# Performance work log

Hardware: AMD Instinct MI355X
Metric: run time of the kernel (lower is better)

Reference implementation:

```python
import jax, jax.numpy as jnp
import numpy as np

N = 100000      # nodes
E = 1600000     # edges (before self-loops)
IN = 128        # in_channels
HID = 64        # hidden_channels
HEADS = 2
G = 64          # graphs in batch
NEG_SLOPE = 0.2


def setup_inputs() -> dict:
    key = jax.random.key(0)
    ks = jax.random.split(key, 13)
    x = jax.random.normal(ks[0], (N, IN), dtype=jnp.float32)
    edge_index = jax.random.randint(ks[1], (2, E), 0, N, dtype=jnp.int64)
    batch = jnp.sort(jax.random.randint(ks[2], (N,), 0, G, dtype=jnp.int64))
    # GATConv 1: in=128 -> 64 per head, heads=2, concat
    W1 = jax.random.normal(ks[3], (IN, HEADS * HID), dtype=jnp.float32) / np.sqrt(IN)
    a1_src = jax.random.normal(ks[4], (HEADS, HID), dtype=jnp.float32) / np.sqrt(HID)
    a1_dst = jax.random.normal(ks[5], (HEADS, HID), dtype=jnp.float32) / np.sqrt(HID)
    b1 = jnp.zeros((HEADS * HID,), dtype=jnp.float32)
    # GATConv 2: in=128 -> 64, heads=1, mean (concat=False)
    W2 = jax.random.normal(ks[6], (HEADS * HID, 1 * HID), dtype=jnp.float32) / np.sqrt(HEADS * HID)
    a2_src = jax.random.normal(ks[7], (1, HID), dtype=jnp.float32) / np.sqrt(HID)
    a2_dst = jax.random.normal(ks[8], (1, HID), dtype=jnp.float32) / np.sqrt(HID)
    b2 = jnp.zeros((HID,), dtype=jnp.float32)
    # final Linear(64, 1)
    Wlin = jax.random.normal(ks[9], (HID, 1), dtype=jnp.float32) / np.sqrt(HID)
    blin = jnp.zeros((1,), dtype=jnp.float32)
    return {"x": x, "edge_index": edge_index, "batch": batch,
            "W1": W1, "a1_src": a1_src, "a1_dst": a1_dst, "b1": b1,
            "W2": W2, "a2_src": a2_src, "a2_dst": a2_dst, "b2": b2,
            "Wlin": Wlin, "blin": blin}


def gat_conv(x, src, dst, W, a_src, a_dst, bias, heads, out_dim, concat):
    # x: [N, F_in]; src/dst: [E'] (self-loops already included, PyG default)
    h = (x @ W).reshape(-1, heads, out_dim)                 # [N, H, C]
    alpha_s = jnp.sum(h * a_src[None], axis=-1)             # [N, H]
    alpha_d = jnp.sum(h * a_dst[None], axis=-1)             # [N, H]
    e = alpha_s[src] + alpha_d[dst]                         # [E', H]
    e = jnp.where(e > 0, e, NEG_SLOPE * e)                  # LeakyReLU(0.2)
    # segment softmax over incoming edges of each destination node
    e_max = jax.ops.segment_max(e, dst, num_segments=N)     # [N, H]
    e_exp = jnp.exp(e - e_max[dst])
    denom = jax.ops.segment_sum(e_exp, dst, num_segments=N) # [N, H]
    alpha = e_exp / denom[dst]                              # [E', H]
    msg = h[src] * alpha[..., None]                         # [E', H, C]
    out = jax.ops.segment_sum(msg, dst, num_segments=N)     # [N, H, C]
    if concat:
        out = out.reshape(-1, heads * out_dim)
    else:
        out = out.mean(axis=1)
    return out + bias


def reference(x, edge_index, batch, W1, a1_src, a1_dst, b1, W2, a2_src, a2_dst, b2, Wlin, blin):
    loops = jnp.arange(N, dtype=edge_index.dtype)
    src = jnp.concatenate([edge_index[0], loops])
    dst = jnp.concatenate([edge_index[1], loops])
    h = gat_conv(x, src, dst, W1, a1_src, a1_dst, b1, HEADS, HID, concat=True)
    h = jax.nn.relu(h)
    h = gat_conv(h, src, dst, W2, a2_src, a2_dst, b2, 1, HID, concat=False)
    h = jax.nn.relu(h)
    # global mean pool over graph ids
    sums = jax.ops.segment_sum(h, batch, num_segments=G)    # [G, HID]
    cnts = jax.ops.segment_sum(jnp.ones((N,), h.dtype), batch, num_segments=G)
    pooled = sums / jnp.maximum(cnts, 1.0)[:, None]
    return pooled @ Wlin + blin                             # [G, 1]
```

## Files before the change

### kernel.cpp

```cpp
#include <hip/hip_runtime.h>
#include <hip/hip_fp16.h>

#define NEG_SLOPE 0.2f
#define BSH 9
#define NBUCK 256
#define NB1 256
#define DCAP 12288

typedef _Float16 f16;
typedef __attribute__((ext_vector_type(8))) _Float16 half8;
typedef __attribute__((ext_vector_type(4))) _Float16 half4;
typedef __attribute__((ext_vector_type(4))) float f32x4;

__global__ __launch_bounds__(128) void prep_w(
    const float* __restrict__ W1, const float* __restrict__ W2,
    f16* __restrict__ W1t, f16* __restrict__ W2t)
{
    int b = blockIdx.x, k = threadIdx.x;
    if (b < 128) W1t[b * 128 + k] = (f16)W1[k * 128 + b];
    else { int c = b - 128; W2t[c * 128 + k] = (f16)W2[k * 64 + c]; }
}

__global__ __launch_bounds__(256) void gemm1_kernel(
    const float* __restrict__ x, const f16* __restrict__ W1t,
    const float* __restrict__ a1s_vec, const float* __restrict__ a1d_vec,
    f16* __restrict__ h1h, float* __restrict__ a1s, float* __restrict__ a1d, int N)
{
    __shared__ f16 Ash[64 * 136];
    __shared__ f16 Bsh[128 * 136];
    int t = threadIdx.x;
    int row0 = blockIdx.x << 6;

    #pragma unroll
    for (int c = 0; c < 8; ++c) {
        int l = c * 256 + t;
        int r = l >> 5, f = l & 31;
        int rr = row0 + r;
        float4 v = {0.f, 0.f, 0.f, 0.f};
        if (rr < N) v = *(const float4*)&x[(size_t)rr * 128 + f * 4];
        half4 hv = {(f16)v.x, (f16)v.y, (f16)v.z, (f16)v.w};
        *(half4*)&Ash[r * 136 + f * 4] = hv;
    }
    #pragma unroll
    for (int c = 0; c < 8; ++c) {
        int l = c * 256 + t;
        int row = l >> 4, f = l & 15;
        *(half8*)&Bsh[row * 136 + f * 8] = *(const half8*)&W1t[row * 128 + f * 8];
    }
    __syncthreads();

    int lane = t & 63, w = t >> 6;
    int lr = lane & 15, kg = lane >> 4;
    f32x4 acc[8];
    #pragma unroll
    for (int ct = 0; ct < 8; ++ct) acc[ct] = (f32x4){0.f, 0.f, 0.f, 0.f};

    #pragma unroll
    for (int kt = 0; kt < 4; ++kt) {
        half8 af = *(const half8*)&Ash[(w * 16 + lr) * 136 + kt * 32 + kg * 8];
        #pragma unroll
        for (int ct = 0; ct < 8; ++ct) {
            half8 bf = *(const half8*)&Bsh[(ct * 16 + lr) * 136 + kt * 32 + kg * 8];
            acc[ct] = __builtin_amdgcn_mfma_f32_16x16x32_f16(af, bf, acc[ct], 0, 0, 0);
        }
    }

    #pragma unroll
    for (int reg = 0; reg < 4; ++reg) {
        float ps0 = 0.f, pd0 = 0.f, ps1 = 0.f, pd1 = 0.f;
        #pragma unroll
        for (int ct = 0; ct < 4; ++ct) {
            float a = acc[ct][reg];
            ps0 += a * a1s_vec[ct * 16 + lr];
            pd0 += a * a1d_vec[ct * 16 + lr];
        }
        #pragma unroll
        for (int ct = 4; ct < 8; ++ct) {
            float a = acc[ct][reg];
            ps1 += a * a1s_vec[ct * 16 + lr];
            pd1 += a * a1d_vec[ct * 16 + lr];
        }
        #pragma unroll
        for (int o = 1; o <= 8; o <<= 1) {
            ps0 += __shfl_xor(ps0, o); pd0 += __shfl_xor(pd0, o);
            ps1 += __shfl_xor(ps1, o); pd1 += __shfl_xor(pd1, o);
        }
        if (lr == 0) {
            int rr = row0 + w * 16 + kg * 4 + reg;
            if (rr < N) {
                a1s[rr * 2] = ps0; a1d[rr * 2] = pd0;
                a1s[rr * 2 + 1] = ps1; a1d[rr * 2 + 1] = pd1;
            }
        }
    }

    __syncthreads();
    #pragma unroll
    for (int ct = 0; ct < 8; ++ct)
        #pragma unroll
        for (int reg = 0; reg < 4; ++reg)
            Ash[(w * 16 + kg * 4 + reg) * 136 + ct * 16 + lr] = (f16)acc[ct][reg];
    __syncthreads();
    #pragma unroll
    for (int c = 0; c < 4; ++c) {
        int l = c * 256 + t;
        int r = l >> 4, f = l & 15;
        int rr = row0 + r;
        if (rr < N) *(half8*)&h1h[(size_t)rr * 128 + f * 8] = *(const half8*)&Ash[r * 136 + f * 8];
    }
}

__global__ __launch_bounds__(256) void bucket_count(
    const int* __restrict__ ei, int* __restrict__ cntg,
    float* __restrict__ poolz, int nz, int E, int Ep, int chunk)
{
    __shared__ int lc[NBUCK];
    int i = blockIdx.x, t = threadIdx.x;
    if (i == 0) for (int z = t; z < nz; z += 256) poolz[z] = 0.f;
    lc[t] = 0;
    __syncthreads();
    int e0 = i * chunk, e1 = min(e0 + chunk, Ep);
    for (int e = e0 + t; e < e1; e += 256) {
        int dst = (e < E) ? ei[E + e] : e - E;
        atomicAdd(&lc[dst >> BSH], 1);
    }
    __syncthreads();
    cntg[i * NBUCK + t] = lc[t];
}

__global__ __launch_bounds__(256) void bucket_scan_t(
    const int* __restrict__ cntg, int* __restrict__ offs, int* __restrict__ tot)
{
    __shared__ int sh[256];
    int b = blockIdx.x, i = threadIdx.x;
    int v = cntg[i * NBUCK + b];
    sh[i] = v;
    __syncthreads();
    for (int off = 1; off < 256; off <<= 1) {
        int u = (i >= off) ? sh[i - off] : 0;
        __syncthreads();
        sh[i] += u;
        __syncthreads();
    }
    offs[i * NBUCK + b] = sh[i] - v;
    if (i == 255) tot[b] = sh[255];
}

__global__ __launch_bounds__(256) void bucket_place(
    const int* __restrict__ ei, const int* __restrict__ offs, const int* __restrict__ tot,
    unsigned* __restrict__ pairs, int E, int Ep, int chunk)
{
    __shared__ int cur[NBUCK];
    __shared__ int sh[256];
    int i = blockIdx.x, t = threadIdx.x;
    int v = tot[t];
    sh[t] = v;
    __syncthreads();
    for (int off = 1; off < 256; off <<= 1) {
        int u = (t >= off) ? sh[t - off] : 0;
        __syncthreads();
        sh[t] += u;
        __syncthreads();
    }
    cur[t] = offs[i * NBUCK + t] + sh[t] - v;
    __syncthreads();
    int e0 = i * chunk, e1 = min(e0 + chunk, Ep);
    for (int e = e0 + t; e < e1; e += 256) {
        int src, dst;
        if (e < E) { src = ei[e]; dst = ei[E + e]; } else { src = dst = e - E; }
        int pos = atomicAdd(&cur[dst >> BSH], 1);
        pairs[pos] = ((unsigned)(dst & 511) << 17) | (unsigned)src;
    }
}

__global__ __launch_bounds__(256) void bucket_build(
    const unsigned* __restrict__ pairs, const int* __restrict__ tot,
    int* __restrict__ rowStart, int* __restrict__ deg, int* __restrict__ srcS, int N)
{
    __shared__ int ucnt[512], ustart[512], sh[256];
    __shared__ unsigned stage[DCAP];
    int b = blockIdx.x, t = threadIdx.x;
    int node0 = b << BSH;
    if (node0 >= N) return;
    ucnt[t] = 0; ucnt[t + 256] = 0;
    int v = tot[t];
    sh[t] = v;
    __syncthreads();
    for (int off = 1; off < 256; off <<= 1) {
        int u = (t >= off) ? sh[t - off] : 0;
        __syncthreads();
        sh[t] += u;
        __syncthreads();
    }
    int s0 = (b == 0) ? 0 : sh[b - 1];
    int s1 = sh[b];
    int cnt = s1 - s0;
    __syncthreads();
    bool fit = (cnt <= DCAP);
    for (int k = t; k < cnt; k += 256) {
        unsigned pv = pairs[s0 + k];
        if (fit) stage[k] = pv;
        atomicAdd(&ucnt[pv >> 17], 1);
    }
    __syncthreads();
    int a0 = ucnt[2 * t], a1 = ucnt[2 * t + 1];
    int s2 = a0 + a1;
    sh[t] = s2;
    __syncthreads();
    for (int off = 1; off < 256; off <<= 1) {
        int u = (t >= off) ? sh[t - off] : 0;
        __syncthreads();
        sh[t] += u;
        __syncthreads();
    }
    int exc = sh[t] - s2;
    ustart[2 * t] = exc;
    ustart[2 * t + 1] = exc + a0;
    __syncthreads();
    for (int l = t; l < 512; l += 256) {
        int node = node0 + l;
        if (node < N) { rowStart[node] = s0 + ustart[l]; deg[node] = ucnt[l]; }
    }
    __syncthreads();
    for (int k = t; k < cnt; k += 256) {
        unsigned pv = fit ? stage[k] : pairs[s0 + k];
        int pos = atomicAdd(&ustart[pv >> 17], 1);
        srcS[s0 + pos] = (int)(pv & 131071u);
    }
}

__global__ __launch_bounds__(256) void fused_aggr1(
    const int* __restrict__ rowStart, const int* __restrict__ deg, const int* __restrict__ srcS,
    const float* __restrict__ a1s, const float* __restrict__ a1d, const float* __restrict__ b1,
    const f16* __restrict__ h1h, f16* __restrict__ out1h, int N)
{
    int lane = threadIdx.x & 63;
    int dst = blockIdx.x * 4 + (threadIdx.x >> 6);
    if (dst >= N) return;
    int base = rowStart[dst];
    int d = deg[dst];
    float ad0 = a1d[2 * dst], ad1 = a1d[2 * dst + 1];
    int tx = lane & 15, j2 = lane >> 4;
    float acc[8] = {};
    float dpart0 = 0.f, dpart1 = 0.f;

    for (int c0 = 0; c0 < d; c0 += 64) {
        int cn = min(64, d - c0);
        int s = 0; float p0 = 0.f, p1 = 0.f;
        if (lane < cn) {
            s = srcS[base + c0 + lane];
            float2 av = *(const float2*)&a1s[2 * s];
            float e0 = av.x + ad0, e1 = av.y + ad1;
            e0 = e0 > 0.f ? e0 : NEG_SLOPE * e0;
            e1 = e1 > 0.f ? e1 : NEG_SLOPE * e1;
            p0 = __expf(e0); p1 = __expf(e1);
        }
        dpart0 += p0; dpart1 += p1;
        int niter = (cn + 3) >> 2;
        #pragma unroll 4
        for (int jj = 0; jj < niter; ++jj) {
            int esub = jj * 4 + j2;
            int   sj = __shfl(s, esub);
            float q0 = __shfl(p0, esub);
            float q1 = __shfl(p1, esub);
            float q  = (tx < 8) ? q0 : q1;
            half8 v = *(const half8*)&h1h[(size_t)sj * 128 + tx * 8];
            #pragma unroll
            for (int k = 0; k < 8; ++k) acc[k] += q * (float)v[k];
        }
    }
    #pragma unroll
    for (int k = 0; k < 8; ++k) acc[k] += __shfl_xor(acc[k], 16);
    #pragma unroll
    for (int k = 0; k < 8; ++k) acc[k] += __shfl_xor(acc[k], 32);
    #pragma unroll
    for (int o = 32; o; o >>= 1) { dpart0 += __shfl_xor(dpart0, o); dpart1 += __shfl_xor(dpart1, o); }
    if (j2 == 0) {
        float iv = (tx < 8) ? (1.f / dpart0) : (1.f / dpart1);
        float4 blo = *(const float4*)&b1[tx * 8];
        float4 bhi = *(const float4*)&b1[tx * 8 + 4];
        float o0 = fmaxf(acc[0] * iv + blo.x, 0.f);
        float o1 = fmaxf(acc[1] * iv + blo.y, 0.f);
        float o2 = fmaxf(acc[2] * iv + blo.z, 0.f);
        float o3 = fmaxf(acc[3] * iv + blo.w, 0.f);
        float o4 = fmaxf(acc[4] * iv + bhi.x, 0.f);
        float o5 = fmaxf(acc[5] * iv + bhi.y, 0.f);
        float o6 = fmaxf(acc[6] * iv + bhi.z, 0.f);
        float o7 = fmaxf(acc[7] * iv + bhi.w, 0.f);
        half8 hv = {(f16)o0, (f16)o1, (f16)o2, (f16)o3, (f16)o4, (f16)o5, (f16)o6, (f16)o7};
        *(half8*)&out1h[(size_t)dst * 128 + tx * 8] = hv;
    }
}

__global__ __launch_bounds__(256) void gemm2_kernel(
    const f16* __restrict__ out1h, const f16* __restrict__ W2t,
    const float* __restrict__ a2s_vec, const float* __restrict__ a2d_vec,
    f16* __restrict__ h2h, float* __restrict__ a2s, float* __restrict__ a2d, int N)
{
    __shared__ f16 Ash[64 * 136];
    __shared__ f16 Bsh[64 * 136];
    int t = threadIdx.x;
    int row0 = blockIdx.x << 6;

    #pragma unroll
    for (int c = 0; c < 4; ++c) {
        int l = c * 256 + t;
        int r = l >> 4, f = l & 15;
        int rr = row0 + r;
        half8 hv = {0, 0, 0, 0, 0, 0, 0, 0};
        if (rr < N) hv = *(const half8*)&out1h[(size_t)rr * 128 + f * 8];
        *(half8*)&Ash[r * 136 + f * 8] = hv;
    }
    #pragma unroll
    for (int c = 0; c < 4; ++c) {
        int l = c * 256 + t;
        int row = l >> 4, f = l & 15;
        *(half8*)&Bsh[row * 136 + f * 8] = *(const half8*)&W2t[row * 128 + f * 8];
    }
    __syncthreads();

    int lane = t & 63, w = t >> 6;
    int lr = lane & 15, kg = lane >> 4;
    f32x4 acc[4];
    #pragma unroll
    for (int ct = 0; ct < 4; ++ct) acc[ct] = (f32x4){0.f, 0.f, 0.f, 0.f};

    #pragma unroll
    for (int kt = 0; kt < 4; ++kt) {
        half8 af = *(const half8*)&Ash[(w * 16 + lr) * 136 + kt * 32 + kg * 8];
        #pragma unroll
        for (int ct = 0; ct < 4; ++ct) {
            half8 bf = *(const half8*)&Bsh[(ct * 16 + lr) * 136 + kt * 32 + kg * 8];
            acc[ct] = __builtin_amdgcn_mfma_f32_16x16x32_f16(af, bf, acc[ct], 0, 0, 0);
        }
    }

    #pragma unroll
    for (int reg = 0; reg < 4; ++reg) {
        float ps = 0.f, pd = 0.f;
        #pragma unroll
        for (int ct = 0; ct < 4; ++ct) {
            float a = acc[ct][reg];
            ps += a * a2s_vec[ct * 16 + lr];
            pd += a * a2d_vec[ct * 16 + lr];
        }
        #pragma unroll
        for (int o = 1; o <= 8; o <<= 1) { ps += __shfl_xor(ps, o); pd += __shfl_xor(pd, o); }
        if (lr == 0) {
            int rr = row0 + w * 16 + kg * 4 + reg;
            if (rr < N) { a2s[rr] = ps; a2d[rr] = pd; }
        }
    }

    __syncthreads();
    #pragma unroll
    for (int ct = 0; ct < 4; ++ct)
        #pragma unroll
        for (int reg = 0; reg < 4; ++reg)
            Ash[(w * 16 + kg * 4 + reg) * 136 + ct * 16 + lr] = (f16)acc[ct][reg];
    __syncthreads();
    #pragma unroll
    for (int c = 0; c < 2; ++c) {
        int l = c * 256 + t;
        int r = l >> 3, f = l & 7;
        int rr = row0 + r;
        if (rr < N) *(half8*)&h2h[(size_t)rr * 64 + f * 8] = *(const half8*)&Ash[r * 136 + f * 8];
    }
}

__global__ __launch_bounds__(256) void fused_aggr2(
    const int* __restrict__ rowStart, const int* __restrict__ deg, const int* __restrict__ srcS,
    const float* __restrict__ a2s, const float* __restrict__ a2d, const float* __restrict__ b2,
    const f16* __restrict__ h2h, f16* __restrict__ out2h, int N)
{
    int lane = threadIdx.x & 63;
    int dst = blockIdx.x * 4 + (threadIdx.x >> 6);
    if (dst >= N) return;
    int base = rowStart[dst];
    int d = deg[dst];
    float ad = a2d[dst];
    int tx = lane & 7, j3 = lane >> 3;
    float acc[8] = {};
    float dpart = 0.f;

    for (int c0 = 0; c0 < d; c0 += 64) {
        int cn = min(64, d - c0);
        int s = 0; float p = 0.f;
        if (lane < cn) {
            s = srcS[base + c0 + lane];
            float e = a2s[s] + ad;
            e = e > 0.f ? e : NEG_SLOPE * e;
            p = __expf(e);
        }
        dpart += p;
        int niter = (cn + 7) >> 3;
        #pragma unroll 4
        for (int jj = 0; jj < niter; ++jj) {
            int esub = jj * 8 + j3;
            int   sj = __shfl(s, esub);
            float q  = __shfl(p, esub);
            half8 v = *(const half8*)&h2h[(size_t)sj * 64 + tx * 8];
            #pragma unroll
            for (int k = 0; k < 8; ++k) acc[k] += q * (float)v[k];
        }
    }
    #pragma unroll
    for (int k = 0; k < 8; ++k) acc[k] += __shfl_xor(acc[k], 8);
    #pragma unroll
    for (int k = 0; k < 8; ++k) acc[k] += __shfl_xor(acc[k], 16);
    #pragma unroll
    for (int k = 0; k < 8; ++k) acc[k] += __shfl_xor(acc[k], 32);
    #pragma unroll
    for (int o = 32; o; o >>= 1) dpart += __shfl_xor(dpart, o);
    if (j3 == 0) {
        float iv = 1.f / dpart;
        float4 blo = *(const float4*)&b2[tx * 8];
        float4 bhi = *(const float4*)&b2[tx * 8 + 4];
        float o0 = fmaxf(acc[0] * iv + blo.x, 0.f);
        float o1 = fmaxf(acc[1] * iv + blo.y, 0.f);
        float o2 = fmaxf(acc[2] * iv + blo.z, 0.f);
        float o3 = fmaxf(acc[3] * iv + blo.w, 0.f);
        float o4 = fmaxf(acc[4] * iv + bhi.x, 0.f);
        float o5 = fmaxf(acc[5] * iv + bhi.y, 0.f);
        float o6 = fmaxf(acc[6] * iv + bhi.z, 0.f);
        float o7 = fmaxf(acc[7] * iv + bhi.w, 0.f);
        half8 hv = {(f16)o0, (f16)o1, (f16)o2, (f16)o3, (f16)o4, (f16)o5, (f16)o6, (f16)o7};
        *(half8*)&out2h[(size_t)dst * 64 + tx * 8] = hv;
    }
}

__global__ __launch_bounds__(256) void pool_kernel(
    const f16* __restrict__ out2h, const int* __restrict__ batch,
    float* __restrict__ pool, float* __restrict__ cnt, int N)
{
    int lane = threadIdx.x & 63;
    int gwave = blockIdx.x * 4 + (threadIdx.x >> 6);
    int nwaves = gridDim.x * 4;
    int per = (N + nwaves - 1) / nwaves;
    int n0 = gwave * per;
    int n1 = min(n0 + per, N);
    if (n0 >= n1) return;
    float acc = 0.f;
    int count = 0;
    int gcur = batch[n0];
    for (int n = n0; n < n1; ++n) {
        int g = batch[n];
        if (g != gcur) {
            atomicAdd(&pool[gcur * 64 + lane], acc);
            if (lane == 0) atomicAdd(&cnt[gcur], (float)count);
            acc = 0.f; count = 0; gcur = g;
        }
        acc += (float)out2h[(size_t)n * 64 + lane];
        ++count;
    }
    atomicAdd(&pool[gcur * 64 + lane], acc);
    if (lane == 0) atomicAdd(&cnt[gcur], (float)count);
}

__global__ void final_kernel(
    const float* __restrict__ pool, const float* __restrict__ cnt,
    const float* __restrict__ Wlin, const float* __restrict__ blin,
    float* __restrict__ out, int G)
{
    int g = threadIdx.x;
    if (g >= G) return;
    float s = 0.f;
    #pragma unroll 8
    for (int c = 0; c < 64; ++c) s += pool[g * 64 + c] * Wlin[c];
    float cn = cnt[g]; cn = cn > 1.f ? cn : 1.f;
    out[g] = s / cn + blin[0];
}

extern "C" void kernel_launch(void* const* d_in, const int* in_sizes, int n_in,
                              void* d_out, int out_size, void* d_ws, size_t ws_size,
                              hipStream_t stream) {
    const float* x     = (const float*)d_in[0];
    const int*   ei    = (const int*)d_in[1];
    const int*   batch = (const int*)d_in[2];
    const float* W1    = (const float*)d_in[3];
    const float* a1sv  = (const float*)d_in[4];
    const float* a1dv  = (const float*)d_in[5];
    const float* b1    = (const float*)d_in[6];
    const float* W2    = (const float*)d_in[7];
    const float* a2sv  = (const float*)d_in[8];
    const float* a2dv  = (const float*)d_in[9];
    const float* b2    = (const float*)d_in[10];
    const float* Wlin  = (const float*)d_in[11];
    const float* blin  = (const float*)d_in[12];

    int N  = in_sizes[2];
    int E  = in_sizes[1] / 2;
    int Ep = E + N;
    const int G = 64;
    int chunk = (Ep + NB1 - 1) / NB1;

    float* ws = (float*)d_ws;
    size_t off = 0;
    f16*  out1h = (f16*)(ws + off); off += (size_t)N * 64;
    f16*  h1h   = (f16*)(ws + off); off += (size_t)N * 64;
    f16*  h2h   = (f16*)(ws + off); off += (size_t)N * 32;
    float* a1s  = ws + off; off += (size_t)N * 2;
    float* a1d  = ws + off; off += (size_t)N * 2;
    float* a2s  = ws + off; off += N;
    float* a2d  = ws + off; off += N;
    int* degA   = (int*)(ws + off); off += N;
    int* rowStart = (int*)(ws + off); off += N;
    int* cntg   = (int*)(ws + off); off += NB1 * NBUCK;
    int* offs   = (int*)(ws + off); off += NB1 * NBUCK;
    int* tot    = (int*)(ws + off); off += NBUCK;
    unsigned* pairs = (unsigned*)(ws + off); off += Ep;
    int* srcS   = (int*)(ws + off); off += Ep;
    float* pool = ws + off; off += G * 64;
    float* cnt  = ws + off; off += G;
    f16* W1t    = (f16*)(ws + off); off += 128 * 64;
    f16* W2t    = (f16*)(ws + off); off += 64 * 64;
    f16* out2h  = h1h;

    prep_w<<<192, 128, 0, stream>>>(W1, W2, W1t, W2t);

    bucket_count<<<NB1, 256, 0, stream>>>(ei, cntg, pool, G * 64 + G, E, Ep, chunk);
    bucket_scan_t<<<NBUCK, 256, 0, stream>>>(cntg, offs, tot);
    bucket_place<<<NB1, 256, 0, stream>>>(ei, offs, tot, pairs, E, Ep, chunk);
    bucket_build<<<NBUCK, 256, 0, stream>>>(pairs, tot, rowStart, degA, srcS, N);

    gemm1_kernel<<<(N + 63) / 64, 256, 0, stream>>>(x, W1t, a1sv, a1dv, h1h, a1s, a1d, N);
    fused_aggr1<<<(N + 3) / 4, 256, 0, stream>>>(rowStart, degA, srcS, a1s, a1d, b1, h1h, out1h, N);
    gemm2_kernel<<<(N + 63) / 64, 256, 0, stream>>>(out1h, W2t, a2sv, a2dv, h2h, a2s, a2d, N);
    fused_aggr2<<<(N + 3) / 4, 256, 0, stream>>>(rowStart, degA, srcS, a2s, a2d, b2, h2h, out2h, N);
    pool_kernel<<<256, 256, 0, stream>>>(out2h, batch, pool, cnt, N);
    final_kernel<<<1, 64, 0, stream>>>(pool, cnt, Wlin, blin, (float*)d_out, G);
}
```

Measured before the change: 264.6 us.

## Merge setup kernels, co-schedule CSR build with GEMM1, fuse pooling into aggregation

Weight transposition and pool zeroing move into the bucket-count kernel. The per-bucket CSR build and the first GEMM share one launch, splitting work by block index over a shared LDS buffer; the staging capacity shrinks to fit. Mean pooling is folded into the second aggregation kernel through atomics into 32 replicated pool buffers, removing the out2h round trip and the separate pool kernel. The final kernel now reduces across the replicas, which adds atomic traffic and makes the summation order nondeterministic.

```diff
diff --git a/kernel.cpp b/kernel.cpp
--- a/kernel.cpp
+++ b/kernel.cpp
@@ -5,31 +5,161 @@
 #define BSH 9
 #define NBUCK 256
 #define NB1 256
-#define DCAP 12288
+#define DCAP 11264
+#define NREP 32
 
 typedef _Float16 f16;
 typedef __attribute__((ext_vector_type(8))) _Float16 half8;
 typedef __attribute__((ext_vector_type(4))) _Float16 half4;
 typedef __attribute__((ext_vector_type(4))) float f32x4;
 
-__global__ __launch_bounds__(128) void prep_w(
+__global__ __launch_bounds__(256) void kernelA(
     const float* __restrict__ W1, const float* __restrict__ W2,
-    f16* __restrict__ W1t, f16* __restrict__ W2t)
-{
-    int b = blockIdx.x, k = threadIdx.x;
-    if (b < 128) W1t[b * 128 + k] = (f16)W1[k * 128 + b];
-    else { int c = b - 128; W2t[c * 128 + k] = (f16)W2[k * 64 + c]; }
-}
-
-__global__ __launch_bounds__(256) void gemm1_kernel(
+    f16* __restrict__ W1t, f16* __restrict__ W2t,
+    const int* __restrict__ ei, int* __restrict__ cntg,
+    float* __restrict__ zbase, int nz, int E, int Ep, int chunk)
+{
+    __shared__ int lc[NBUCK];
+    int b = blockIdx.x, t = threadIdx.x;
+    if (b < 64) {
+        int k = t & 127, c = 2 * b + (t >> 7);
+        W1t[c * 128 + k] = (f16)W1[k * 128 + c];
+        return;
+    }
+    if (b < 96) {
+        int k = t & 127, c = 2 * (b - 64) + (t >> 7);
+        W2t[c * 128 + k] = (f16)W2[k * 64 + c];
+        return;
+    }
+    int i = b - 96;
+    int per = (nz + NB1 - 1) / NB1;
+    for (int z = i * per + t; z < min((i + 1) * per, nz); z += 256) zbase[z] = 0.f;
+    lc[t] = 0;
+    __syncthreads();
+    int e0 = i * chunk, e1 = min(e0 + chunk, Ep);
+    for (int e = e0 + t; e < e1; e += 256) {
+        int dst = (e < E) ? ei[E + e] : e - E;
+        atomicAdd(&lc[dst >> BSH], 1);
+    }
+    __syncthreads();
+    cntg[i * NBUCK + t] = lc[t];
+}
+
+__global__ __launch_bounds__(256) void bucket_scan_t(
+    const int* __restrict__ cntg, int* __restrict__ offs, int* __restrict__ tot)
+{
+    __shared__ int sh[256];
+    int b = blockIdx.x, i = threadIdx.x;
+    int v = cntg[i * NBUCK + b];
+    sh[i] = v;
+    __syncthreads();
+    for (int off = 1; off < 256; off <<= 1) {
+        int u = (i >= off) ? sh[i - off] : 0;
+        __syncthreads();
+        sh[i] += u;
+        __syncthreads();
+    }
+    offs[i * NBUCK + b] = sh[i] - v;
+    if (i == 255) tot[b] = sh[255];
+}
+
+__global__ __launch_bounds__(256) void bucket_place(
+    const int* __restrict__ ei, const int* __restrict__ offs, const int* __restrict__ tot,
+    unsigned* __restrict__ pairs, int E, int Ep, int chunk)
+{
+    __shared__ int cur[NBUCK];
+    __shared__ int sh[256];
+    int i = blockIdx.x, t = threadIdx.x;
+    int v = tot[t];
+    sh[t] = v;
+    __syncthreads();
+    for (int off = 1; off < 256; off <<= 1) {
+        int u = (t >= off) ? sh[t - off] : 0;
+        __syncthreads();
+        sh[t] += u;
+        __syncthreads();
+    }
+    cur[t] = offs[i * NBUCK + t] + sh[t] - v;
+    __syncthreads();
+    int e0 = i * chunk, e1 = min(e0 + chunk, Ep);
+    for (int e = e0 + t; e < e1; e += 256) {
+        int src, dst;
+        if (e < E) { src = ei[e]; dst = ei[E + e]; } else { src = dst = e - E; }
+        int pos = atomicAdd(&cur[dst >> BSH], 1);
+        pairs[pos] = ((unsigned)(dst & 511) << 17) | (unsigned)src;
+    }
+}
+
+#define SMEM_BYTES 52224
+__global__ __launch_bounds__(256) void kernelB(
+    const unsigned* __restrict__ pairs, const int* __restrict__ tot,
+    int* __restrict__ rowStart, int* __restrict__ deg, int* __restrict__ srcS,
     const float* __restrict__ x, const f16* __restrict__ W1t,
     const float* __restrict__ a1s_vec, const float* __restrict__ a1d_vec,
     f16* __restrict__ h1h, float* __restrict__ a1s, float* __restrict__ a1d, int N)
 {
-    __shared__ f16 Ash[64 * 136];
-    __shared__ f16 Bsh[128 * 136];
+    __shared__ char smem[SMEM_BYTES];
     int t = threadIdx.x;
-    int row0 = blockIdx.x << 6;
+
+    if (blockIdx.x < NBUCK) {
+        int* ucnt = (int*)smem;
+        int* ustart = ucnt + 512;
+        int* sh = ustart + 512;
+        unsigned* stage = (unsigned*)(sh + 256);
+        int b = blockIdx.x;
+        int node0 = b << BSH;
+        if (node0 >= N) return;
+        ucnt[t] = 0; ucnt[t + 256] = 0;
+        int v = tot[t];
+        sh[t] = v;
+        __syncthreads();
+        for (int off = 1; off < 256; off <<= 1) {
+            int u = (t >= off) ? sh[t - off] : 0;
+            __syncthreads();
+            sh[t] += u;
+            __syncthreads();
+        }
+        int s0 = (b == 0) ? 0 : sh[b - 1];
+        int s1 = sh[b];
+        int cnt = s1 - s0;
+        __syncthreads();
+        bool fit = (cnt <= DCAP);
+        for (int k = t; k < cnt; k += 256) {
+            unsigned pv = pairs[s0 + k];
+            if (fit) stage[k] = pv;
+            atomicAdd(&ucnt[pv >> 17], 1);
+        }
+        __syncthreads();
+        int a0 = ucnt[2 * t], a1 = ucnt[2 * t + 1];
+        int s2 = a0 + a1;
+        sh[t] = s2;
+        __syncthreads();
+        for (int off = 1; off < 256; off <<= 1) {
+            int u = (t >= off) ? sh[t - off] : 0;
+            __syncthreads();
+            sh[t] += u;
+            __syncthreads();
+        }
+        int exc = sh[t] - s2;
+        ustart[2 * t] = exc;
+        ustart[2 * t + 1] = exc + a0;
+        __syncthreads();
+        for (int l = t; l < 512; l += 256) {
+            int node = node0 + l;
+            if (node < N) { rowStart[node] = s0 + ustart[l]; deg[node] = ucnt[l]; }
+        }
+        __syncthreads();
+        for (int k = t; k < cnt; k += 256) {
+            unsigned pv = fit ? stage[k] : pairs[s0 + k];
+            int pos = atomicAdd(&ustart[pv >> 17], 1);
+            srcS[s0 + pos] = (int)(pv & 131071u);
+        }
+        return;
+    }
+
+    f16* Ash = (f16*)smem;
+    f16* Bsh = Ash + 64 * 136;
+    int row0 = (blockIdx.x - NBUCK) << 6;
 
     #pragma unroll
     for (int c = 0; c < 8; ++c) {
@@ -107,125 +237,6 @@
         int r = l >> 4, f = l & 15;
         int rr = row0 + r;
         if (rr < N) *(half8*)&h1h[(size_t)rr * 128 + f * 8] = *(const half8*)&Ash[r * 136 + f * 8];
-    }
-}
-
-__global__ __launch_bounds__(256) void bucket_count(
-    const int* __restrict__ ei, int* __restrict__ cntg,
-    float* __restrict__ poolz, int nz, int E, int Ep, int chunk)
-{
-    __shared__ int lc[NBUCK];
-    int i = blockIdx.x, t = threadIdx.x;
-    if (i == 0) for (int z = t; z < nz; z += 256) poolz[z] = 0.f;
-    lc[t] = 0;
-    __syncthreads();
-    int e0 = i * chunk, e1 = min(e0 + chunk, Ep);
-    for (int e = e0 + t; e < e1; e += 256) {
-        int dst = (e < E) ? ei[E + e] : e - E;
-        atomicAdd(&lc[dst >> BSH], 1);
-    }
-    __syncthreads();
-    cntg[i * NBUCK + t] = lc[t];
-}
-
-__global__ __launch_bounds__(256) void bucket_scan_t(
-    const int* __restrict__ cntg, int* __restrict__ offs, int* __restrict__ tot)
-{
-    __shared__ int sh[256];
-    int b = blockIdx.x, i = threadIdx.x;
-    int v = cntg[i * NBUCK + b];
-    sh[i] = v;
-    __syncthreads();
-    for (int off = 1; off < 256; off <<= 1) {
-        int u = (i >= off) ? sh[i - off] : 0;
-        __syncthreads();
-        sh[i] += u;
-        __syncthreads();
-    }
-    offs[i * NBUCK + b] = sh[i] - v;
-    if (i == 255) tot[b] = sh[255];
-}
-
-__global__ __launch_bounds__(256) void bucket_place(
-    const int* __restrict__ ei, const int* __restrict__ offs, const int* __restrict__ tot,
-    unsigned* __restrict__ pairs, int E, int Ep, int chunk)
-{
-    __shared__ int cur[NBUCK];
-    __shared__ int sh[256];
-    int i = blockIdx.x, t = threadIdx.x;
-    int v = tot[t];
-    sh[t] = v;
-    __syncthreads();
-    for (int off = 1; off < 256; off <<= 1) {
-        int u = (t >= off) ? sh[t - off] : 0;
-        __syncthreads();
-        sh[t] += u;
-        __syncthreads();
-    }
-    cur[t] = offs[i * NBUCK + t] + sh[t] - v;
-    __syncthreads();
-    int e0 = i * chunk, e1 = min(e0 + chunk, Ep);
-    for (int e = e0 + t; e < e1; e += 256) {
-        int src, dst;
-        if (e < E) { src = ei[e]; dst = ei[E + e]; } else { src = dst = e - E; }
-        int pos = atomicAdd(&cur[dst >> BSH], 1);
-        pairs[pos] = ((unsigned)(dst & 511) << 17) | (unsigned)src;
-    }
-}
-
-__global__ __launch_bounds__(256) void bucket_build(
-    const unsigned* __restrict__ pairs, const int* __restrict__ tot,
-    int* __restrict__ rowStart, int* __restrict__ deg, int* __restrict__ srcS, int N)
-{
-    __shared__ int ucnt[512], ustart[512], sh[256];
-    __shared__ unsigned stage[DCAP];
-    int b = blockIdx.x, t = threadIdx.x;
-    int node0 = b << BSH;
-    if (node0 >= N) return;
-    ucnt[t] = 0; ucnt[t + 256] = 0;
-    int v = tot[t];
-    sh[t] = v;
-    __syncthreads();
-    for (int off = 1; off < 256; off <<= 1) {
-        int u = (t >= off) ? sh[t - off] : 0;
-        __syncthreads();
-        sh[t] += u;
-        __syncthreads();
-    }
-    int s0 = (b == 0) ? 0 : sh[b - 1];
-    int s1 = sh[b];
-    int cnt = s1 - s0;
-    __syncthreads();
-    bool fit = (cnt <= DCAP);
-    for (int k = t; k < cnt; k += 256) {
-        unsigned pv = pairs[s0 + k];
-        if (fit) stage[k] = pv;
-        atomicAdd(&ucnt[pv >> 17], 1);
-    }
-    __syncthreads();
-    int a0 = ucnt[2 * t], a1 = ucnt[2 * t + 1];
-    int s2 = a0 + a1;
-    sh[t] = s2;
-    __syncthreads();
-    for (int off = 1; off < 256; off <<= 1) {
-        int u = (t >= off) ? sh[t - off] : 0;
-        __syncthreads();
-        sh[t] += u;
-        __syncthreads();
-    }
-    int exc = sh[t] - s2;
-    ustart[2 * t] = exc;
-    ustart[2 * t + 1] = exc + a0;
-    __syncthreads();
-    for (int l = t; l < 512; l += 256) {
-        int node = node0 + l;
-        if (node < N) { rowStart[node] = s0 + ustart[l]; deg[node] = ucnt[l]; }
-    }
-    __syncthreads();
-    for (int k = t; k < cnt; k += 256) {
-        unsigned pv = fit ? stage[k] : pairs[s0 + k];
-        int pos = atomicAdd(&ustart[pv >> 17], 1);
-        srcS[s0 + pos] = (int)(pv & 131071u);
     }
 }
 
@@ -371,7 +382,8 @@
 __global__ __launch_bounds__(256) void fused_aggr2(
     const int* __restrict__ rowStart, const int* __restrict__ deg, const int* __restrict__ srcS,
     const float* __restrict__ a2s, const float* __restrict__ a2d, const float* __restrict__ b2,
-    const f16* __restrict__ h2h, f16* __restrict__ out2h, int N)
+    const f16* __restrict__ h2h, const int* __restrict__ batch,
+    float* __restrict__ poolrep, float* __restrict__ cntrep, int N)
 {
     int lane = threadIdx.x & 63;
     int dst = blockIdx.x * 4 + (threadIdx.x >> 6);
@@ -416,59 +428,42 @@
         float iv = 1.f / dpart;
         float4 blo = *(const float4*)&b2[tx * 8];
         float4 bhi = *(const float4*)&b2[tx * 8 + 4];
-        float o0 = fmaxf(acc[0] * iv + blo.x, 0.f);
-        float o1 = fmaxf(acc[1] * iv + blo.y, 0.f);
-        float o2 = fmaxf(acc[2] * iv + blo.z, 0.f);
-        float o3 = fmaxf(acc[3] * iv + blo.w, 0.f);
-        float o4 = fmaxf(acc[4] * iv + bhi.x, 0.f);
-        float o5 = fmaxf(acc[5] * iv + bhi.y, 0.f);
-        float o6 = fmaxf(acc[6] * iv + bhi.z, 0.f);
-        float o7 = fmaxf(acc[7] * iv + bhi.w, 0.f);
-        half8 hv = {(f16)o0, (f16)o1, (f16)o2, (f16)o3, (f16)o4, (f16)o5, (f16)o6, (f16)o7};
-        *(half8*)&out2h[(size_t)dst * 64 + tx * 8] = hv;
-    }
-}
-
-__global__ __launch_bounds__(256) void pool_kernel(
-    const f16* __restrict__ out2h, const int* __restrict__ batch,
-    float* __restrict__ pool, float* __restrict__ cnt, int N)
-{
-    int lane = threadIdx.x & 63;
-    int gwave = blockIdx.x * 4 + (threadIdx.x >> 6);
-    int nwaves = gridDim.x * 4;
-    int per = (N + nwaves - 1) / nwaves;
-    int n0 = gwave * per;
-    int n1 = min(n0 + per, N);
-    if (n0 >= n1) return;
-    float acc = 0.f;
-    int count = 0;
-    int gcur = batch[n0];
-    for (int n = n0; n < n1; ++n) {
-        int g = batch[n];
-        if (g != gcur) {
-            atomicAdd(&pool[gcur * 64 + lane], acc);
-            if (lane == 0) atomicAdd(&cnt[gcur], (float)count);
-            acc = 0.f; count = 0; gcur = g;
-        }
-        acc += (float)out2h[(size_t)n * 64 + lane];
-        ++count;
-    }
-    atomicAdd(&pool[gcur * 64 + lane], acc);
-    if (lane == 0) atomicAdd(&cnt[gcur], (float)count);
-}
-
-__global__ void final_kernel(
-    const float* __restrict__ pool, const float* __restrict__ cnt,
+        float o_[8];
+        o_[0] = fmaxf(acc[0] * iv + blo.x, 0.f);
+        o_[1] = fmaxf(acc[1] * iv + blo.y, 0.f);
+        o_[2] = fmaxf(acc[2] * iv + blo.z, 0.f);
+        o_[3] = fmaxf(acc[3] * iv + blo.w, 0.f);
+        o_[4] = fmaxf(acc[4] * iv + bhi.x, 0.f);
+        o_[5] = fmaxf(acc[5] * iv + bhi.y, 0.f);
+        o_[6] = fmaxf(acc[6] * iv + bhi.z, 0.f);
+        o_[7] = fmaxf(acc[7] * iv + bhi.w, 0.f);
+        int g = batch[dst];
+        float* pb = &poolrep[(blockIdx.x & (NREP - 1)) * (64 * 64) + g * 64 + tx * 8];
+        #pragma unroll
+        for (int k = 0; k < 8; ++k) atomicAdd(&pb[k], o_[k]);
+        if (tx == 0) atomicAdd(&cntrep[(blockIdx.x & (NREP - 1)) * 64 + g], 1.0f);
+    }
+}
+
+__global__ __launch_bounds__(64) void final_kernel(
+    const float* __restrict__ poolrep, const float* __restrict__ cntrep,
     const float* __restrict__ Wlin, const float* __restrict__ blin,
     float* __restrict__ out, int G)
 {
-    int g = threadIdx.x;
-    if (g >= G) return;
+    int g = blockIdx.x, c = threadIdx.x;
     float s = 0.f;
-    #pragma unroll 8
-    for (int c = 0; c < 64; ++c) s += pool[g * 64 + c] * Wlin[c];
-    float cn = cnt[g]; cn = cn > 1.f ? cn : 1.f;
-    out[g] = s / cn + blin[0];
+    #pragma unroll
+    for (int r = 0; r < NREP; ++r) s += poolrep[r * (64 * 64) + g * 64 + c];
+    s *= Wlin[c];
+    #pragma unroll
+    for (int o = 32; o; o >>= 1) s += __shfl_xor(s, o);
+    if (c == 0) {
+        float cn = 0.f;
+        #pragma unroll
+        for (int r = 0; r < NREP; ++r) cn += cntrep[r * 64 + g];
+        cn = cn > 1.f ? cn : 1.f;
+        out[g] = s / cn + blin[0];
+    }
 }
 
 extern "C" void kernel_launch(void* const* d_in, const int* in_sizes, int n_in,
@@ -510,23 +505,21 @@
     int* tot    = (int*)(ws + off); off += NBUCK;
     unsigned* pairs = (unsigned*)(ws + off); off += Ep;
     int* srcS   = (int*)(ws + off); off += Ep;
-    float* pool = ws + off; off += G * 64;
-    float* cnt  = ws + off; off += G;
+    float* poolrep = ws + off; off += NREP * 64 * 64;
+    float* cntrep  = ws + off; off += NREP * 64;
     f16* W1t    = (f16*)(ws + off); off += 128 * 64;
     f16* W2t    = (f16*)(ws + off); off += 64 * 64;
-    f16* out2h  = h1h;
-
-    prep_w<<<192, 128, 0, stream>>>(W1, W2, W1t, W2t);
-
-    bucket_count<<<NB1, 256, 0, stream>>>(ei, cntg, pool, G * 64 + G, E, Ep, chunk);
+
+    int nzero = NREP * 64 * 64 + NREP * 64;
+
+    kernelA<<<96 + NB1, 256, 0, stream>>>(W1, W2, W1t, W2t, ei, cntg, poolrep, nzero, E, Ep, chunk);
     bucket_scan_t<<<NBUCK, 256, 0, stream>>>(cntg, offs, tot);
     bucket_place<<<NB1, 256, 0, stream>>>(ei, offs, tot, pairs, E, Ep, chunk);
-    bucket_build<<<NBUCK, 256, 0, stream>>>(pairs, tot, rowStart, degA, srcS, N);
-
-    gemm1_kernel<<<(N + 63) / 64, 256, 0, stream>>>(x, W1t, a1sv, a1dv, h1h, a1s, a1d, N);
+    kernelB<<<NBUCK + (N + 63) / 64, 256, 0, stream>>>(
+        pairs, tot, rowStart, degA, srcS,
+        x, W1t, a1sv, a1dv, h1h, a1s, a1d, N);
     fused_aggr1<<<(N + 3) / 4, 256, 0, stream>>>(rowStart, degA, srcS, a1s, a1d, b1, h1h, out1h, N);
     gemm2_kernel<<<(N + 63) / 64, 256, 0, stream>>>(out1h, W2t, a2sv, a2dv, h2h, a2s, a2d, N);
-    fused_aggr2<<<(N + 3) / 4, 256, 0, stream>>>(rowStart, degA, srcS, a2s, a2d, b2, h2h, out2h, N);
-    pool_kernel<<<256, 256, 0, stream>>>(out2h, batch, pool, cnt, N);
-    final_kernel<<<1, 64, 0, stream>>>(pool, cnt, Wlin, blin, (float*)d_out, G);
-}
+    fused_aggr2<<<(N + 3) / 4, 256, 0, stream>>>(rowStart, degA, srcS, a2s, a2d, b2, h2h, batch, poolrep, cntrep, N);
+    final_kernel<<<G, 64, 0, stream>>>(poolrep, cntrep, Wlin, blin, (float*)d_out, G);
+}
```

New measurement: 714.0 us. +169.9%, slower.

## Merge weight prep with bucket count and CSR build with first GEMM

Applied to the files above, without the earlier changes.

Weight transposition now runs in the same launch as edge bucket counting, and the per-bucket CSR build runs in the same launch as the first GEMM, with block ranges picking the role. Shared memory becomes a single union buffer, and DCAP shrinks so the build staging fits inside the GEMM's allocation. The aim is to remove two kernel launches and let independent work overlap on the GPU. In exchange, buckets larger than the smaller DCAP fall back to global reads, and the kernels now mix heterogeneous blocks that share one shared-memory footprint.

```diff
diff --git a/kernel.cpp b/kernel.cpp
--- a/kernel.cpp
+++ b/kernel.cpp
@@ -5,31 +5,159 @@
 #define BSH 9
 #define NBUCK 256
 #define NB1 256
-#define DCAP 12288
+#define DCAP 11264
 
 typedef _Float16 f16;
 typedef __attribute__((ext_vector_type(8))) _Float16 half8;
 typedef __attribute__((ext_vector_type(4))) _Float16 half4;
 typedef __attribute__((ext_vector_type(4))) float f32x4;
 
-__global__ __launch_bounds__(128) void prep_w(
+__global__ __launch_bounds__(256) void kernelA(
     const float* __restrict__ W1, const float* __restrict__ W2,
-    f16* __restrict__ W1t, f16* __restrict__ W2t)
-{
-    int b = blockIdx.x, k = threadIdx.x;
-    if (b < 128) W1t[b * 128 + k] = (f16)W1[k * 128 + b];
-    else { int c = b - 128; W2t[c * 128 + k] = (f16)W2[k * 64 + c]; }
-}
-
-__global__ __launch_bounds__(256) void gemm1_kernel(
+    f16* __restrict__ W1t, f16* __restrict__ W2t,
+    const int* __restrict__ ei, int* __restrict__ cntg,
+    float* __restrict__ zbase, int nz, int E, int Ep, int chunk)
+{
+    __shared__ int lc[NBUCK];
+    int b = blockIdx.x, t = threadIdx.x;
+    if (b < 64) {
+        int k = t & 127, c = 2 * b + (t >> 7);
+        W1t[c * 128 + k] = (f16)W1[k * 128 + c];
+        return;
+    }
+    if (b < 96) {
+        int k = t & 127, c = 2 * (b - 64) + (t >> 7);
+        W2t[c * 128 + k] = (f16)W2[k * 64 + c];
+        return;
+    }
+    int i = b - 96;
+    if (i == 0) for (int z = t; z < nz; z += 256) zbase[z] = 0.f;
+    lc[t] = 0;
+    __syncthreads();
+    int e0 = i * chunk, e1 = min(e0 + chunk, Ep);
+    for (int e = e0 + t; e < e1; e += 256) {
+        int dst = (e < E) ? ei[E + e] : e - E;
+        atomicAdd(&lc[dst >> BSH], 1);
+    }
+    __syncthreads();
+    cntg[i * NBUCK + t] = lc[t];
+}
+
+__global__ __launch_bounds__(256) void bucket_scan_t(
+    const int* __restrict__ cntg, int* __restrict__ offs, int* __restrict__ tot)
+{
+    __shared__ int sh[256];
+    int b = blockIdx.x, i = threadIdx.x;
+    int v = cntg[i * NBUCK + b];
+    sh[i] = v;
+    __syncthreads();
+    for (int off = 1; off < 256; off <<= 1) {
+        int u = (i >= off) ? sh[i - off] : 0;
+        __syncthreads();
+        sh[i] += u;
+        __syncthreads();
+    }
+    offs[i * NBUCK + b] = sh[i] - v;
+    if (i == 255) tot[b] = sh[255];
+}
+
+__global__ __launch_bounds__(256) void bucket_place(
+    const int* __restrict__ ei, const int* __restrict__ offs, const int* __restrict__ tot,
+    unsigned* __restrict__ pairs, int E, int Ep, int chunk)
+{
+    __shared__ int cur[NBUCK];
+    __shared__ int sh[256];
+    int i = blockIdx.x, t = threadIdx.x;
+    int v = tot[t];
+    sh[t] = v;
+    __syncthreads();
+    for (int off = 1; off < 256; off <<= 1) {
+        int u = (t >= off) ? sh[t - off] : 0;
+        __syncthreads();
+        sh[t] += u;
+        __syncthreads();
+    }
+    cur[t] = offs[i * NBUCK + t] + sh[t] - v;
+    __syncthreads();
+    int e0 = i * chunk, e1 = min(e0 + chunk, Ep);
+    for (int e = e0 + t; e < e1; e += 256) {
+        int src, dst;
+        if (e < E) { src = ei[e]; dst = ei[E + e]; } else { src = dst = e - E; }
+        int pos = atomicAdd(&cur[dst >> BSH], 1);
+        pairs[pos] = ((unsigned)(dst & 511) << 17) | (unsigned)src;
+    }
+}
+
+#define SMEM_BYTES 52224
+__global__ __launch_bounds__(256) void kernelB(
+    const unsigned* __restrict__ pairs, const int* __restrict__ tot,
+    int* __restrict__ rowStart, int* __restrict__ deg, int* __restrict__ srcS,
     const float* __restrict__ x, const f16* __restrict__ W1t,
     const float* __restrict__ a1s_vec, const float* __restrict__ a1d_vec,
     f16* __restrict__ h1h, float* __restrict__ a1s, float* __restrict__ a1d, int N)
 {
-    __shared__ f16 Ash[64 * 136];
-    __shared__ f16 Bsh[128 * 136];
+    __shared__ char smem[SMEM_BYTES];
     int t = threadIdx.x;
-    int row0 = blockIdx.x << 6;
+
+    if (blockIdx.x < NBUCK) {
+        int* ucnt = (int*)smem;
+        int* ustart = ucnt + 512;
+        int* sh = ustart + 512;
+        unsigned* stage = (unsigned*)(sh + 256);
+        int b = blockIdx.x;
+        int node0 = b << BSH;
+        if (node0 >= N) return;
+        ucnt[t] = 0; ucnt[t + 256] = 0;
+        int v = tot[t];
+        sh[t] = v;
+        __syncthreads();
+        for (int off = 1; off < 256; off <<= 1) {
+            int u = (t >= off) ? sh[t - off] : 0;
+            __syncthreads();
+            sh[t] += u;
+            __syncthreads();
+        }
+        int s0 = (b == 0) ? 0 : sh[b - 1];
+        int s1 = sh[b];
+        int cnt = s1 - s0;
+        __syncthreads();
+        bool fit = (cnt <= DCAP);
+        for (int k = t; k < cnt; k += 256) {
+            unsigned pv = pairs[s0 + k];
+            if (fit) stage[k] = pv;
+            atomicAdd(&ucnt[pv >> 17], 1);
+        }
+        __syncthreads();
+        int a0 = ucnt[2 * t], a1 = ucnt[2 * t + 1];
+        int s2 = a0 + a1;
+        sh[t] = s2;
+        __syncthreads();
+        for (int off = 1; off < 256; off <<= 1) {
+            int u = (t >= off) ? sh[t - off] : 0;
+            __syncthreads();
+            sh[t] += u;
+            __syncthreads();
+        }
+        int exc = sh[t] - s2;
+        ustart[2 * t] = exc;
+        ustart[2 * t + 1] = exc + a0;
+        __syncthreads();
+        for (int l = t; l < 512; l += 256) {
+            int node = node0 + l;
+            if (node < N) { rowStart[node] = s0 + ustart[l]; deg[node] = ucnt[l]; }
+        }
+        __syncthreads();
+        for (int k = t; k < cnt; k += 256) {
+            unsigned pv = fit ? stage[k] : pairs[s0 + k];
+            int pos = atomicAdd(&ustart[pv >> 17], 1);
+            srcS[s0 + pos] = (int)(pv & 131071u);
+        }
+        return;
+    }
+
+    f16* Ash = (f16*)smem;
+    f16* Bsh = Ash + 64 * 136;
+    int row0 = (blockIdx.x - NBUCK) << 6;
 
     #pragma unroll
     for (int c = 0; c < 8; ++c) {
@@ -107,125 +235,6 @@
         int r = l >> 4, f = l & 15;
         int rr = row0 + r;
         if (rr < N) *(half8*)&h1h[(size_t)rr * 128 + f * 8] = *(const half8*)&Ash[r * 136 + f * 8];
-    }
-}
-
-__global__ __launch_bounds__(256) void bucket_count(
-    const int* __restrict__ ei, int* __restrict__ cntg,
-    float* __restrict__ poolz, int nz, int E, int Ep, int chunk)
-{
-    __shared__ int lc[NBUCK];
-    int i = blockIdx.x, t = threadIdx.x;
-    if (i == 0) for (int z = t; z < nz; z += 256) poolz[z] = 0.f;
-    lc[t] = 0;
-    __syncthreads();
-    int e0 = i * chunk, e1 = min(e0 + chunk, Ep);
-    for (int e = e0 + t; e < e1; e += 256) {
-        int dst = (e < E) ? ei[E + e] : e - E;
-        atomicAdd(&lc[dst >> BSH], 1);
-    }
-    __syncthreads();
-    cntg[i * NBUCK + t] = lc[t];
-}
-
-__global__ __launch_bounds__(256) void bucket_scan_t(
-    const int* __restrict__ cntg, int* __restrict__ offs, int* __restrict__ tot)
-{
-    __shared__ int sh[256];
-    int b = blockIdx.x, i = threadIdx.x;
-    int v = cntg[i * NBUCK + b];
-    sh[i] = v;
-    __syncthreads();
-    for (int off = 1; off < 256; off <<= 1) {
-        int u = (i >= off) ? sh[i - off] : 0;
-        __syncthreads();
-        sh[i] += u;
-        __syncthreads();
-    }
-    offs[i * NBUCK + b] = sh[i] - v;
-    if (i == 255) tot[b] = sh[255];
-}
-
-__global__ __launch_bounds__(256) void bucket_place(
-    const int* __restrict__ ei, const int* __restrict__ offs, const int* __restrict__ tot,
-    unsigned* __restrict__ pairs, int E, int Ep, int chunk)
-{
-    __shared__ int cur[NBUCK];
-    __shared__ int sh[256];
-    int i = blockIdx.x, t = threadIdx.x;
-    int v = tot[t];
-    sh[t] = v;
-    __syncthreads();
-    for (int off = 1; off < 256; off <<= 1) {
-        int u = (t >= off) ? sh[t - off] : 0;
-        __syncthreads();
-        sh[t] += u;
-        __syncthreads();
-    }
-    cur[t] = offs[i * NBUCK + t] + sh[t] - v;
-    __syncthreads();
-    int e0 = i * chunk, e1 = min(e0 + chunk, Ep);
-    for (int e = e0 + t; e < e1; e += 256) {
-        int src, dst;
-        if (e < E) { src = ei[e]; dst = ei[E + e]; } else { src = dst = e - E; }
-        int pos = atomicAdd(&cur[dst >> BSH], 1);
-        pairs[pos] = ((unsigned)(dst & 511) << 17) | (unsigned)src;
-    }
-}
-
-__global__ __launch_bounds__(256) void bucket_build(
-    const unsigned* __restrict__ pairs, const int* __restrict__ tot,
-    int* __restrict__ rowStart, int* __restrict__ deg, int* __restrict__ srcS, int N)
-{
-    __shared__ int ucnt[512], ustart[512], sh[256];
-    __shared__ unsigned stage[DCAP];
-    int b = blockIdx.x, t = threadIdx.x;
-    int node0 = b << BSH;
-    if (node0 >= N) return;
-    ucnt[t] = 0; ucnt[t + 256] = 0;
-    int v = tot[t];
-    sh[t] = v;
-    __syncthreads();
-    for (int off = 1; off < 256; off <<= 1) {
-        int u = (t >= off) ? sh[t - off] : 0;
-        __syncthreads();
-        sh[t] += u;
-        __syncthreads();
-    }
-    int s0 = (b == 0) ? 0 : sh[b - 1];
-    int s1 = sh[b];
-    int cnt = s1 - s0;
-    __syncthreads();
-    bool fit = (cnt <= DCAP);
-    for (int k = t; k < cnt; k += 256) {
-        unsigned pv = pairs[s0 + k];
-        if (fit) stage[k] = pv;
-        atomicAdd(&ucnt[pv >> 17], 1);
-    }
-    __syncthreads();
-    int a0 = ucnt[2 * t], a1 = ucnt[2 * t + 1];
-    int s2 = a0 + a1;
-    sh[t] = s2;
-    __syncthreads();
-    for (int off = 1; off < 256; off <<= 1) {
-        int u = (t >= off) ? sh[t - off] : 0;
-        __syncthreads();
-        sh[t] += u;
-        __syncthreads();
-    }
-    int exc = sh[t] - s2;
-    ustart[2 * t] = exc;
-    ustart[2 * t + 1] = exc + a0;
-    __syncthreads();
-    for (int l = t; l < 512; l += 256) {
-        int node = node0 + l;
-        if (node < N) { rowStart[node] = s0 + ustart[l]; deg[node] = ucnt[l]; }
-    }
-    __syncthreads();
-    for (int k = t; k < cnt; k += 256) {
-        unsigned pv = fit ? stage[k] : pairs[s0 + k];
-        int pos = atomicAdd(&ustart[pv >> 17], 1);
-        srcS[s0 + pos] = (int)(pv & 131071u);
     }
 }
 
@@ -516,14 +525,12 @@
     f16* W2t    = (f16*)(ws + off); off += 64 * 64;
     f16* out2h  = h1h;
 
-    prep_w<<<192, 128, 0, stream>>>(W1, W2, W1t, W2t);
-
-    bucket_count<<<NB1, 256, 0, stream>>>(ei, cntg, pool, G * 64 + G, E, Ep, chunk);
+    kernelA<<<96 + NB1, 256, 0, stream>>>(W1, W2, W1t, W2t, ei, cntg, pool, G * 64 + G, E, Ep, chunk);
     bucket_scan_t<<<NBUCK, 256, 0, stream>>>(cntg, offs, tot);
     bucket_place<<<NB1, 256, 0, stream>>>(ei, offs, tot, pairs, E, Ep, chunk);
-    bucket_build<<<NBUCK, 256, 0, stream>>>(pairs, tot, rowStart, degA, srcS, N);
-
-    gemm1_kernel<<<(N + 63) / 64, 256, 0, stream>>>(x, W1t, a1sv, a1dv, h1h, a1s, a1d, N);
+    kernelB<<<NBUCK + (N + 63) / 64, 256, 0, stream>>>(
+        pairs, tot, rowStart, degA, srcS,
+        x, W1t, a1sv, a1dv, h1h, a1s, a1d, N);
     fused_aggr1<<<(N + 3) / 4, 256, 0, stream>>>(rowStart, degA, srcS, a1s, a1d, b1, h1h, out1h, N);
     gemm2_kernel<<<(N + 63) / 64, 256, 0, stream>>>(out1h, W2t, a2sv, a2dv, h2h, a2s, a2d, N);
     fused_aggr2<<<(N + 3) / 4, 256, 0, stream>>>(rowStart, degA, srcS, a2s, a2d, b2, h2h, out2h, N);
```

Result: faster. 241.3 us (-8.8%).
